# Optimization experiments

Measured on AMD Instinct MI355X. Metric: run time of the kernel, lower is better.

Reference implementation:

```python
import jax, jax.numpy as jnp
import numpy as np

N_FFT = 2048
STRIDE = 512
FREQ_BINS = N_FFT  # __init__ passes freq_bins=n_fft


def _fourier_kernels():
    s = np.arange(N_FFT, dtype=np.float64)
    # scipy get_window('hann', n_fft, fftbins=True)
    win = 0.5 - 0.5 * np.cos(2.0 * np.pi * s / N_FFT)
    k = np.arange(FREQ_BINS, dtype=np.float64)
    phase = 2.0 * np.pi * np.outer(k, s) / N_FFT  # (bins, n_fft)
    wsin = (win * np.sin(phase)).astype(np.float32)
    wcos = (win * np.cos(phase)).astype(np.float32)
    return wsin, wcos


def setup_inputs() -> dict:
    key = jax.random.key(0)
    x = jax.random.normal(key, (8, 262144), dtype=jnp.float32)
    wsin, wcos = _fourier_kernels()
    return {"x": x, "wsin": jnp.asarray(wsin), "wcos": jnp.asarray(wcos)}


def reference(x, wsin, wcos):
    # center=True, pad_mode='reflect'
    xp = jnp.pad(x, ((0, 0), (N_FFT // 2, N_FFT // 2)), mode="reflect")
    num_frames = (xp.shape[1] - N_FFT) // STRIDE + 1
    # frame the signal: (batch, num_frames, n_fft)
    idx = np.arange(num_frames)[:, None] * STRIDE + np.arange(N_FFT)
    frames = xp[:, idx]
    # dense DFT as GEMM (equivalent to conv1d with sin/cos filters)
    imag = jnp.einsum("btn,kn->bkt", frames, wsin)
    real = jnp.einsum("btn,kn->bkt", frames, wcos)
    return (real, -imag)
```

## Files before the change

kernel.cpp:

```cpp
#include <hip/hip_runtime.h>
#include <hip/hip_bf16.h>
#include <stdint.h>
#include <math.h>

#define XLEN   262144
#define NT     513
#define NTP    528
#define NB     8
#define NCOL   (NB * NTP)
#define PROW   256
#define KQ     512
#define NK     1088
#define NFFT   2048
#define OUTKT  (2048 * NT)
#define WSTR   ((size_t)PROW * KQ)
#define FSTR   ((size_t)NCOL * KQ)
#define PSTR   ((size_t)PROW * NCOL)
#define NWG4   528

typedef __attribute__((ext_vector_type(8))) short short8;
typedef __attribute__((ext_vector_type(4))) short short4v;
typedef __attribute__((ext_vector_type(2))) short short2v;
typedef __attribute__((ext_vector_type(4))) float f32x4;

__device__ __forceinline__ short cvt_bf16(float f) {
  return __builtin_bit_cast(short, (__bf16)f);
}

__device__ __forceinline__ f32x4 bf4_to_f32(short4v v) {
  f32x4 o;
#pragma unroll
  for (int e = 0; e < 4; ++e) {
    uint32_t u = ((uint32_t)(uint16_t)v[e]) << 16;
    o[e] = __builtin_bit_cast(float, u);
  }
  return o;
}

__device__ __forceinline__ void gload16(const short* g, const short* l) {
  __builtin_amdgcn_global_load_lds(
      (const __attribute__((address_space(1))) void*)g,
      (__attribute__((address_space(3))) void*)l, 16, 0, 0);
}


__global__ __launch_bounds__(256) void conv_prep4(
    const float* __restrict__ x,
    const float* __restrict__ wsin, const float* __restrict__ wcos,
    short* __restrict__ wc4, short* __restrict__ ws4,
    short* __restrict__ fr4, float* __restrict__ Tbuf) {
  const int tid = threadIdx.x;
  const int n0 = tid * 8;
  const int m0 = n0 >> 2;
  if (blockIdx.x < PROW) {
    const int row = blockIdx.x;
    short2v c[4], s[4];
    const float* pc = wcos + (size_t)row * NFFT + n0;
    const float* ps = wsin + (size_t)row * NFFT + n0;
    f32x4 c0 = *(const f32x4*)pc, c1 = *(const f32x4*)(pc + 4);
    f32x4 s0 = *(const f32x4*)ps, s1 = *(const f32x4*)(ps + 4);
#pragma unroll
    for (int r = 0; r < 4; ++r) {
      c[r][0] = cvt_bf16(c0[r]); c[r][1] = cvt_bf16(c1[r]);
      s[r][0] = cvt_bf16(s0[r]); s[r][1] = cvt_bf16(s1[r]);
    }
    const size_t o = (size_t)row * KQ + m0;
#pragma unroll
    for (int r = 0; r < 4; ++r) {
      *(short2v*)&wc4[r * WSTR + o] = c[r];
      *(short2v*)&ws4[r * WSTR + o] = s[r];
    }
  } else {
    const int j = blockIdx.x - PROW;
    const int b = j / NTP;
    const int t = j - b * NTP;
    short2v v[4];
    float con[4] = {0.f, 0.f, 0.f, 0.f};
    if (t < NT) {
      const float* xb = x + (size_t)b * XLEN;
      const int q0 = t * 512 + n0 - 1024;
      float f[8];
      if (q0 >= 0 && q0 + 7 < XLEN) {
        *(f32x4*)(f)     = *(const f32x4*)(xb + q0);
        *(f32x4*)(f + 4) = *(const f32x4*)(xb + q0 + 4);
      } else {
#pragma unroll
        for (int e = 0; e < 8; ++e) {
          int mm = q0 + e;
          mm = (mm < 0) ? -mm : mm;
          mm = (mm >= XLEN) ? (2 * XLEN - 2 - mm) : mm;
          f[e] = xb[mm];
        }
      }
      float wn[8];
#pragma unroll
      for (int e = 0; e < 8; ++e)
        wn[e] = 0.5f - 0.5f * cosf((float)(M_PI / 1024.0) * (float)(n0 + e));
#pragma unroll
      for (int r = 0; r < 4; ++r) {
        v[r][0] = cvt_bf16(f[r]); v[r][1] = cvt_bf16(f[4 + r]);
        con[r] = wn[r] * f[r] - wn[4 + r] * f[4 + r];
      }
    } else {
#pragma unroll
      for (int r = 0; r < 4; ++r) { v[r][0] = 0; v[r][1] = 0; }
    }
#pragma unroll
    for (int r = 0; r < 4; ++r)
      *(short2v*)&fr4[r * FSTR + (size_t)j * KQ + m0] = v[r];

    const int lane = tid & 63;
    const int wid  = tid >> 6;
#pragma unroll
    for (int r = 0; r < 4; ++r)
#pragma unroll
      for (int off = 32; off >= 1; off >>= 1)
        con[r] += __shfl_down(con[r], off);
    __shared__ float tred[4][4];
    if (lane == 0) {
#pragma unroll
      for (int r = 0; r < 4; ++r) tred[wid][r] = con[r];
    }
    __syncthreads();
    if (tid < 4)
      Tbuf[(size_t)j * 4 + tid] =
          tred[0][tid] + tred[1][tid] + tred[2][tid] + tred[3][tid];
  }
}

__global__ __launch_bounds__(256, 3) void dft_gemm_split4(
    const short* __restrict__ wc4, const short* __restrict__ ws4,
    const short* __restrict__ fr4,
    short* __restrict__ pC4, short* __restrict__ pS4) {
  __shared__ short lds[16384];

  const int tid  = threadIdx.x;
  const int lane = tid & 63;
  const int wid  = tid >> 6;

  const int o   = blockIdx.x;
  const int xcd = o & 7;
  const int wg  = xcd * 66 + (o >> 3);
  const int side = wg / 132;
  const int w    = wg - side * 132;
  const int k0   = (w % 4) * 64;
  const int j0   = (w / 4) * 128;

  const short* Ac = wc4 + side * WSTR;
  const short* As = ws4 + side * WSTR;
  const short* Bf = fr4 + side * FSTR;
  short* pC = pC4 + side * PSTR;
  short* pS = pS4 + side * PSTR;

  const int wrow = (wid >> 1) * 32;
  const int wcol = (wid & 1) * 64;

  f32x4 accC[2][4], accS[2][4];
#pragma unroll
  for (int m = 0; m < 2; ++m)
#pragma unroll
    for (int n = 0; n < 4; ++n) { accC[m][n] = (f32x4)0.0f; accS[m][n] = (f32x4)0.0f; }

  const int fr_r = lane & 15;
  const int srow = lane >> 3;
  const int scol = ((lane & 7) ^ srow) * 8;

  auto stage = [&](int n0) {
#pragma unroll
    for (int i2 = 0; i2 < 8; ++i2) {
      const int q = wid * 8 + i2;
      const short* src;
      int dst;
      if (q < 8) {
        src = Ac + (size_t)(k0 + q * 8 + srow) * KQ + n0 + scol;
        dst = q * 512;
      } else if (q < 16) {
        src = As + (size_t)(k0 + (q - 8) * 8 + srow) * KQ + n0 + scol;
        dst = 4096 + (q - 8) * 512;
      } else {
        src = Bf + (size_t)(j0 + (q - 16) * 8 + srow) * KQ + n0 + scol;
        dst = 8192 + (q - 16) * 512;
      }
      gload16(src, &lds[dst]);
    }
  };

  for (int ts = 0; ts < 8; ++ts) {
    if (ts) __syncthreads();
    stage(ts * 64);
    __syncthreads();
#pragma unroll
    for (int ks = 0; ks < 2; ++ks) {
      const int cc = ks * 4 + (lane >> 4);
      short8 aC[2], aS[2], bF[4];
#pragma unroll
      for (int m = 0; m < 2; ++m) {
        const int r = wrow + m * 16 + fr_r;
        const int off = (r << 6) + ((cc ^ (r & 7)) << 3);
        aC[m] = *(const short8*)&lds[off];
        aS[m] = *(const short8*)&lds[4096 + off];
      }
#pragma unroll
      for (int n = 0; n < 4; ++n) {
        const int r = wcol + n * 16 + fr_r;
        const int off = (r << 6) + ((cc ^ (r & 7)) << 3);
        bF[n] = *(const short8*)&lds[8192 + off];
      }
#pragma unroll
      for (int m = 0; m < 2; ++m)
#pragma unroll
        for (int n = 0; n < 4; ++n) {
          accC[m][n] = __builtin_amdgcn_mfma_f32_16x16x32_bf16(aC[m], bF[n], accC[m][n], 0, 0, 0);
          accS[m][n] = __builtin_amdgcn_mfma_f32_16x16x32_bf16(aS[m], bF[n], accS[m][n], 0, 0, 0);
        }
    }
  }

#pragma unroll
  for (int m = 0; m < 2; ++m) {
    const int row = k0 + wrow + m * 16 + (lane >> 4) * 4;
#pragma unroll
    for (int n = 0; n < 4; ++n) {
      const int col = j0 + wcol + n * 16 + (lane & 15);
      const size_t base = (size_t)row * NCOL + col;
#pragma unroll
      for (int r = 0; r < 4; ++r) {
        pC[base + (size_t)r * NCOL] = cvt_bf16(accC[m][n][r]);
        pS[base + (size_t)r * NCOL] = cvt_bf16(accS[m][n][r]);
      }
    }
  }
}

__global__ __launch_bounds__(256) void combine4_kernel(
    const short* __restrict__ pC4, const short* __restrict__ pS4,
    const float* __restrict__ Tbuf,
    float* __restrict__ outR, float* __restrict__ outI) {
  const int k  = blockIdx.y;
  const int jq = blockIdx.x * 256 + threadIdx.x;
  if (jq >= NCOL / 4) return;
  const int j = jq * 4;
  const int b = j / NTP;
  const int t = j - b * NTP;
  const float RT2 = 0.70710678118654752f;
  f32x4 C[4], S[4];
  if (k == 256) {
    const float ct8[4] = {1.f, RT2, 0.f, -RT2};
    const float st8[4] = {0.f, RT2, 1.f, RT2};
#pragma unroll
    for (int e = 0; e < 4; ++e) {
      f32x4 tj = *(const f32x4*)&Tbuf[(size_t)(j + e) * 4];
#pragma unroll
      for (int r = 0; r < 4; ++r) {
        C[r][e] = ct8[r] * tj[r];
        S[r][e] = st8[r] * tj[r];
      }
    }
  } else {
    const size_t pb = (size_t)k * NCOL + j;
#pragma unroll
    for (int r = 0; r < 4; ++r) {
      C[r] = bf4_to_f32(*(const short4v*)&pC4[r * PSTR + pb]);
      S[r] = bf4_to_f32(*(const short4v*)&pS4[r * PSTR + pb]);
    }
  }
  const f32x4 CA = C[0] + C[2], CB = C[1] + C[3];
  const f32x4 CmA = C[0] - C[2], CmB = C[1] - C[3];
  const f32x4 SA = S[0] + S[2], SB = S[1] + S[3];
  const f32x4 SmA = S[0] - S[2], SmB = S[1] - S[3];

  f32x4 Cw[4], Sw[4];
  Cw[0] = CA + CB;   Sw[0] = SA + SB;
  Cw[1] = CmA - SmB; Sw[1] = SmA + CmB;
  Cw[2] = CA - CB;   Sw[2] = SA - SB;
  Cw[3] = CmA + SmB; Sw[3] = SmA - CmB;

  const size_t ob = (size_t)b * OUTKT + t;
  const bool mir = (k >= 1) && (k <= 255);
#pragma unroll
  for (int jj = 0; jj < 4; ++jj) {
    const int rowD = 512 * jj + k;
    float* rD = outR + ob + (size_t)rowD * NT;
    float* iD = outI + ob + (size_t)rowD * NT;
    const int rowM = 512 * (4 - jj) - k;
    float* rM = outR + ob + (size_t)rowM * NT;
    float* iM = outI + ob + (size_t)rowM * NT;
#pragma unroll
    for (int e = 0; e < 4; ++e) {
      if (t + e < NT) {
        rD[e] = Cw[jj][e];
        iD[e] = -Sw[jj][e];
        if (mir) { rM[e] = Cw[jj][e]; iM[e] = Sw[jj][e]; }
      }
    }
  }
}


__global__ __launch_bounds__(256) void conv_w_kernel(const float* __restrict__ wsin,
                                                     const float* __restrict__ wcos,
                                                     short* __restrict__ wc,
                                                     short* __restrict__ ws) {
  const int row = blockIdx.x;
  const int c = threadIdx.x * 8;
  const float* src = (blockIdx.y ? wsin : wcos) + (size_t)row * NFFT + c;
  short* dst = (blockIdx.y ? ws : wc) + (size_t)row * NFFT + c;
  f32x4 a = *(const f32x4*)src;
  f32x4 b = *(const f32x4*)(src + 4);
  short8 o;
#pragma unroll
  for (int j = 0; j < 4; ++j) { o[j] = cvt_bf16(a[j]); o[4 + j] = cvt_bf16(b[j]); }
  *(short8*)dst = o;
}

__global__ __launch_bounds__(256) void conv_frames_kernel(const float* __restrict__ x,
                                                          short* __restrict__ fr) {
  const int j = blockIdx.x;
  const int b = j / NTP;
  const int t = j - b * NTP;
  const int c = threadIdx.x * 8;
  short8 o;
  if (t >= NT) {
#pragma unroll
    for (int k = 0; k < 8; ++k) o[k] = 0;
  } else {
    const float* xb = x + (size_t)b * XLEN;
    const int base = t * 512 + c - 1024;
    float v[8];
    if (base >= 0 && base + 7 < XLEN) {
      *(f32x4*)(v)     = *(const f32x4*)(xb + base);
      *(f32x4*)(v + 4) = *(const f32x4*)(xb + base + 4);
    } else {
#pragma unroll
      for (int k = 0; k < 8; ++k) {
        int m = base + k;
        m = (m < 0) ? -m : m;
        m = (m >= XLEN) ? (2 * XLEN - 2 - m) : m;
        v[k] = xb[m];
      }
    }
#pragma unroll
    for (int k = 0; k < 8; ++k) o[k] = cvt_bf16(v[k]);
  }
  *(short8*)&fr[(size_t)j * NFFT + c] = o;
}

__global__ __launch_bounds__(256, 3) void dft_gemm_r4(
    const short* __restrict__ wc_bf,
    const short* __restrict__ ws_bf,
    const short* __restrict__ fr_bf,
    float* __restrict__ outR,
    float* __restrict__ outI) {
  __shared__ short lds[16384];

  const int tid  = threadIdx.x;
  const int lane = tid & 63;
  const int wid  = tid >> 6;

  const int o   = blockIdx.x;
  const int xcd = o & 7;
  const int wg  = ((xcd < 1) ? xcd * 71 : 71 + (xcd - 1) * 70) + (o >> 3);
  const int k0  = (wg % 17) * 64;
  const int j0  = (wg / 17) * 128;

  const int wrow = (wid >> 1) * 32;
  const int wcol = (wid & 1) * 64;

  f32x4 accR[2][4], accI[2][4];
#pragma unroll
  for (int m = 0; m < 2; ++m)
#pragma unroll
    for (int n = 0; n < 4; ++n) { accR[m][n] = (f32x4)0.0f; accI[m][n] = (f32x4)0.0f; }

  const int fr_r = lane & 15;
  const int srow = lane >> 3;
  const int scol = ((lane & 7) ^ srow) * 8;

  auto stage = [&](int n0) {
#pragma unroll
    for (int i = 0; i < 8; ++i) {
      const int q = wid * 8 + i;
      const short* src;
      int dst;
      if (q < 8) {
        src = wc_bf + (size_t)(k0 + q * 8 + srow) * NFFT + n0 + scol;
        dst = q * 512;
      } else if (q < 16) {
        src = ws_bf + (size_t)(k0 + (q - 8) * 8 + srow) * NFFT + n0 + scol;
        dst = 4096 + (q - 8) * 512;
      } else {
        src = fr_bf + (size_t)(j0 + (q - 16) * 8 + srow) * NFFT + n0 + scol;
        dst = 8192 + (q - 16) * 512;
      }
      gload16(src, &lds[dst]);
    }
  };

  for (int t = 0; t < 32; ++t) {
    if (t) __syncthreads();
    stage(t * 64);
    __syncthreads();
#pragma unroll
    for (int ks = 0; ks < 2; ++ks) {
      const int cc = ks * 4 + (lane >> 4);
      short8 a_c[2], a_s[2], b_f[4];
#pragma unroll
      for (int m = 0; m < 2; ++m) {
        const int r = wrow + m * 16 + fr_r;
        const int off = (r << 6) + ((cc ^ (r & 7)) << 3);
        a_c[m] = *(const short8*)&lds[off];
        a_s[m] = *(const short8*)&lds[4096 + off];
      }
#pragma unroll
      for (int n = 0; n < 4; ++n) {
        const int r = wcol + n * 16 + fr_r;
        const int off = (r << 6) + ((cc ^ (r & 7)) << 3);
        b_f[n] = *(const short8*)&lds[8192 + off];
      }
#pragma unroll
      for (int m = 0; m < 2; ++m)
#pragma unroll
        for (int n = 0; n < 4; ++n) {
          accR[m][n] = __builtin_amdgcn_mfma_f32_16x16x32_bf16(a_c[m], b_f[n], accR[m][n], 0, 0, 0);
          accI[m][n] = __builtin_amdgcn_mfma_f32_16x16x32_bf16(a_s[m], b_f[n], accI[m][n], 0, 0, 0);
        }
    }
  }

#pragma unroll
  for (int m = 0; m < 2; ++m) {
    const int k = k0 + wrow + m * 16 + (lane >> 4) * 4;
#pragma unroll
    for (int n = 0; n < 4; ++n) {
      const int j = j0 + wcol + n * 16 + (lane & 15);
      const int b = j / NTP;
      const int t = j - b * NTP;
      if (t < NT) {
        const size_t base = (size_t)b * OUTKT + (size_t)k * NT + t;
#pragma unroll
        for (int r = 0; r < 4; ++r) {
          const int kk = k + r;
          const float vr = accR[m][n][r];
          const float vi = accI[m][n][r];
          outR[base + (size_t)r * NT] = vr;
          outI[base + (size_t)r * NT] = -vi;
          if (kk >= 1 && kk <= 960) {
            const size_t mb = (size_t)b * OUTKT + (size_t)(2048 - kk) * NT + t;
            outR[mb] = vr;
            outI[mb] = vi;
          }
        }
      }
    }
  }
}


extern "C" void kernel_launch(void* const* d_in, const int* in_sizes, int n_in,
                              void* d_out, int out_size, void* d_ws, size_t ws_size,
                              hipStream_t stream) {
  const float* x    = (const float*)d_in[0];
  const float* wsin = (const float*)d_in[1];
  const float* wcos = (const float*)d_in[2];
  float* outR = (float*)d_out;
  float* outI = outR + (size_t)NB * OUTKT;

  const size_t need4 = (8 * WSTR + 4 * FSTR + 8 * PSTR) * sizeof(short)
                     + (size_t)NCOL * 4 * sizeof(float);

  if (ws_size >= need4) {
    short* wc4 = (short*)d_ws;
    short* ws4 = wc4 + 4 * WSTR;
    short* fr4 = ws4 + 4 * WSTR;
    short* pC4 = fr4 + 4 * FSTR;
    short* pS4 = pC4 + 4 * PSTR;
    float* Tbuf = (float*)(pS4 + 4 * PSTR);

    conv_prep4<<<PROW + NCOL, 256, 0, stream>>>(x, wsin, wcos, wc4, ws4, fr4, Tbuf);
    dft_gemm_split4<<<NWG4, 256, 0, stream>>>(wc4, ws4, fr4, pC4, pS4);
    combine4_kernel<<<dim3(5, 257), 256, 0, stream>>>(pC4, pS4, Tbuf, outR, outI);
  } else {
    short* wc_bf = (short*)d_ws;
    short* ws_bf = wc_bf + (size_t)NK * NFFT;
    short* fr_bf = ws_bf + (size_t)NK * NFFT;
    conv_w_kernel<<<dim3(NK, 2), 256, 0, stream>>>(wsin, wcos, wc_bf, ws_bf);
    conv_frames_kernel<<<NCOL, 256, 0, stream>>>(x, fr_bf);
    dft_gemm_r4<<<561, 256, 0, stream>>>(wc_bf, ws_bf, fr_bf, outR, outI);
  }
}
```

Before: 57.51 us.

## Fuse combine pass into GEMM via last-arriver atomic ticket per tile group

Removes the separate combine kernel. Each GEMM workgroup increments a per-tile-group counter after writing its partials, and the fourth (last) of the four side workgroups for that tile runs the radix-4 combine and writes the output. This saves one kernel launch and lets combine work overlap with the GEMMs still running, at the cost of threadfences, atomics, and a serialized combine tail on the last-arriving workgroups. Counters are reset in the prep kernel.

```diff
diff --git a/kernel.cpp b/kernel.cpp
--- a/kernel.cpp
+++ b/kernel.cpp
@@ -17,6 +17,7 @@
 #define FSTR   ((size_t)NCOL * KQ)
 #define PSTR   ((size_t)PROW * NCOL)
 #define NWG4   528
+#define NGRP   132
 
 typedef __attribute__((ext_vector_type(8))) short short8;
 typedef __attribute__((ext_vector_type(4))) short short4v;
@@ -43,15 +44,79 @@
       (__attribute__((address_space(3))) void*)l, 16, 0, 0);
 }
 
+__device__ __forceinline__ void combine_item(
+    int k, int jq, const short* __restrict__ pC4, const short* __restrict__ pS4,
+    const float* __restrict__ Tbuf,
+    float* __restrict__ outR, float* __restrict__ outI) {
+  if (jq >= NCOL / 4) return;
+  const int j = jq * 4;
+  const int b = j / NTP;
+  const int t = j - b * NTP;
+  const float RT2 = 0.70710678118654752f;
+  f32x4 C[4], S[4];
+  if (k == 256) {
+    const float ct8[4] = {1.f, RT2, 0.f, -RT2};
+    const float st8[4] = {0.f, RT2, 1.f, RT2};
+#pragma unroll
+    for (int e = 0; e < 4; ++e) {
+      f32x4 tj = *(const f32x4*)&Tbuf[(size_t)(j + e) * 4];
+#pragma unroll
+      for (int r = 0; r < 4; ++r) {
+        C[r][e] = ct8[r] * tj[r];
+        S[r][e] = st8[r] * tj[r];
+      }
+    }
+  } else {
+    const size_t pb = (size_t)k * NCOL + j;
+#pragma unroll
+    for (int r = 0; r < 4; ++r) {
+      C[r] = bf4_to_f32(*(const short4v*)&pC4[r * PSTR + pb]);
+      S[r] = bf4_to_f32(*(const short4v*)&pS4[r * PSTR + pb]);
+    }
+  }
+  const f32x4 CA = C[0] + C[2], CB = C[1] + C[3];
+  const f32x4 CmA = C[0] - C[2], CmB = C[1] - C[3];
+  const f32x4 SA = S[0] + S[2], SB = S[1] + S[3];
+  const f32x4 SmA = S[0] - S[2], SmB = S[1] - S[3];
+
+  f32x4 Cw[4], Sw[4];
+  Cw[0] = CA + CB;   Sw[0] = SA + SB;
+  Cw[1] = CmA - SmB; Sw[1] = SmA + CmB;
+  Cw[2] = CA - CB;   Sw[2] = SA - SB;
+  Cw[3] = CmA + SmB; Sw[3] = SmA - CmB;
+
+  const size_t ob = (size_t)b * OUTKT + t;
+  const bool mir = (k >= 1) && (k <= 255);
+#pragma unroll
+  for (int jj = 0; jj < 4; ++jj) {
+    const int rowD = 512 * jj + k;
+    float* rD = outR + ob + (size_t)rowD * NT;
+    float* iD = outI + ob + (size_t)rowD * NT;
+    const int rowM = 512 * (4 - jj) - k;
+    float* rM = outR + ob + (size_t)rowM * NT;
+    float* iM = outI + ob + (size_t)rowM * NT;
+#pragma unroll
+    for (int e = 0; e < 4; ++e) {
+      if (t + e < NT) {
+        rD[e] = Cw[jj][e];
+        iD[e] = -Sw[jj][e];
+        if (mir) { rM[e] = Cw[jj][e]; iM[e] = Sw[jj][e]; }
+      }
+    }
+  }
+}
+
 
 __global__ __launch_bounds__(256) void conv_prep4(
     const float* __restrict__ x,
     const float* __restrict__ wsin, const float* __restrict__ wcos,
     short* __restrict__ wc4, short* __restrict__ ws4,
-    short* __restrict__ fr4, float* __restrict__ Tbuf) {
+    short* __restrict__ fr4, float* __restrict__ Tbuf,
+    int* __restrict__ cnt) {
   const int tid = threadIdx.x;
   const int n0 = tid * 8;
   const int m0 = n0 >> 2;
+  if (blockIdx.x == 0 && tid < NGRP) cnt[tid] = 0;
   if (blockIdx.x < PROW) {
     const int row = blockIdx.x;
     short2v c[4], s[4];
@@ -131,7 +196,9 @@
 __global__ __launch_bounds__(256, 3) void dft_gemm_split4(
     const short* __restrict__ wc4, const short* __restrict__ ws4,
     const short* __restrict__ fr4,
-    short* __restrict__ pC4, short* __restrict__ pS4) {
+    short* __restrict__ pC4, short* __restrict__ pS4,
+    const float* __restrict__ Tbuf, int* __restrict__ cnt,
+    float* __restrict__ outR, float* __restrict__ outI) {
   __shared__ short lds[16384];
 
   const int tid  = threadIdx.x;
@@ -143,8 +210,10 @@
   const int wg  = xcd * 66 + (o >> 3);
   const int side = wg / 132;
   const int w    = wg - side * 132;
-  const int k0   = (w % 4) * 64;
+  const int kt   = w % 4;
+  const int k0   = kt * 64;
   const int j0   = (w / 4) * 128;
+  const int grp  = kt * 33 + (w / 4);
 
   const short* Ac = wc4 + side * WSTR;
   const short* As = ws4 + side * WSTR;
@@ -230,70 +299,20 @@
       }
     }
   }
-}
-
-__global__ __launch_bounds__(256) void combine4_kernel(
-    const short* __restrict__ pC4, const short* __restrict__ pS4,
-    const float* __restrict__ Tbuf,
-    float* __restrict__ outR, float* __restrict__ outI) {
-  const int k  = blockIdx.y;
-  const int jq = blockIdx.x * 256 + threadIdx.x;
-  if (jq >= NCOL / 4) return;
-  const int j = jq * 4;
-  const int b = j / NTP;
-  const int t = j - b * NTP;
-  const float RT2 = 0.70710678118654752f;
-  f32x4 C[4], S[4];
-  if (k == 256) {
-    const float ct8[4] = {1.f, RT2, 0.f, -RT2};
-    const float st8[4] = {0.f, RT2, 1.f, RT2};
-#pragma unroll
-    for (int e = 0; e < 4; ++e) {
-      f32x4 tj = *(const f32x4*)&Tbuf[(size_t)(j + e) * 4];
-#pragma unroll
-      for (int r = 0; r < 4; ++r) {
-        C[r][e] = ct8[r] * tj[r];
-        S[r][e] = st8[r] * tj[r];
-      }
-    }
-  } else {
-    const size_t pb = (size_t)k * NCOL + j;
-#pragma unroll
-    for (int r = 0; r < 4; ++r) {
-      C[r] = bf4_to_f32(*(const short4v*)&pC4[r * PSTR + pb]);
-      S[r] = bf4_to_f32(*(const short4v*)&pS4[r * PSTR + pb]);
-    }
-  }
-  const f32x4 CA = C[0] + C[2], CB = C[1] + C[3];
-  const f32x4 CmA = C[0] - C[2], CmB = C[1] - C[3];
-  const f32x4 SA = S[0] + S[2], SB = S[1] + S[3];
-  const f32x4 SmA = S[0] - S[2], SmB = S[1] - S[3];
-
-  f32x4 Cw[4], Sw[4];
-  Cw[0] = CA + CB;   Sw[0] = SA + SB;
-  Cw[1] = CmA - SmB; Sw[1] = SmA + CmB;
-  Cw[2] = CA - CB;   Sw[2] = SA - SB;
-  Cw[3] = CmA + SmB; Sw[3] = SmA - CmB;
-
-  const size_t ob = (size_t)b * OUTKT + t;
-  const bool mir = (k >= 1) && (k <= 255);
-#pragma unroll
-  for (int jj = 0; jj < 4; ++jj) {
-    const int rowD = 512 * jj + k;
-    float* rD = outR + ob + (size_t)rowD * NT;
-    float* iD = outI + ob + (size_t)rowD * NT;
-    const int rowM = 512 * (4 - jj) - k;
-    float* rM = outR + ob + (size_t)rowM * NT;
-    float* iM = outI + ob + (size_t)rowM * NT;
-#pragma unroll
-    for (int e = 0; e < 4; ++e) {
-      if (t + e < NT) {
-        rD[e] = Cw[jj][e];
-        iD[e] = -Sw[jj][e];
-        if (mir) { rM[e] = Cw[jj][e]; iM[e] = Sw[jj][e]; }
-      }
-    }
-  }
+
+  __threadfence();
+  __shared__ int ticket;
+  if (tid == 0) ticket = atomicAdd(&cnt[grp], 1);
+  __syncthreads();
+  if (ticket != 3) return;
+  __threadfence();
+
+  const int jq0 = j0 >> 2;
+  for (int item = tid; item < 64 * 32; item += 256)
+    combine_item(k0 + (item >> 5), jq0 + (item & 31), pC4, pS4, Tbuf, outR, outI);
+  if (kt == 3)
+    for (int item = tid; item < 32; item += 256)
+      combine_item(256, jq0 + item, pC4, pS4, Tbuf, outR, outI);
 }
 
 
@@ -466,7 +485,7 @@
   float* outI = outR + (size_t)NB * OUTKT;
 
   const size_t need4 = (8 * WSTR + 4 * FSTR + 8 * PSTR) * sizeof(short)
-                     + (size_t)NCOL * 4 * sizeof(float);
+                     + (size_t)NCOL * 4 * sizeof(float) + NGRP * sizeof(int);
 
   if (ws_size >= need4) {
     short* wc4 = (short*)d_ws;
@@ -475,10 +494,10 @@
     short* pC4 = fr4 + 4 * FSTR;
     short* pS4 = pC4 + 4 * PSTR;
     float* Tbuf = (float*)(pS4 + 4 * PSTR);
-
-    conv_prep4<<<PROW + NCOL, 256, 0, stream>>>(x, wsin, wcos, wc4, ws4, fr4, Tbuf);
-    dft_gemm_split4<<<NWG4, 256, 0, stream>>>(wc4, ws4, fr4, pC4, pS4);
-    combine4_kernel<<<dim3(5, 257), 256, 0, stream>>>(pC4, pS4, Tbuf, outR, outI);
+    int*   cnt  = (int*)(Tbuf + (size_t)NCOL * 4);
+
+    conv_prep4<<<PROW + NCOL, 256, 0, stream>>>(x, wsin, wcos, wc4, ws4, fr4, Tbuf, cnt);
+    dft_gemm_split4<<<NWG4, 256, 0, stream>>>(wc4, ws4, fr4, pC4, pS4, Tbuf, cnt, outR, outI);
   } else {
     short* wc_bf = (short*)d_ws;
     short* ws_bf = wc_bf + (size_t)NK * NFFT;
```

After: 226.5 us. 294% more time.
